# Kernel optimization log

Hardware: AMD Instinct MI355X
Metric: run time of the kernel (lower is better)

Reference implementation:

```python
import jax, jax.numpy as jnp
import numpy as np

N_EXPERTS = 256
N_GROUPS = 8
TOPK_GROUPS = 4
TOPK = 8
ROUTE_SCALE = 2.5
DIM = 7168


def setup_inputs() -> dict:
    key = jax.random.key(0)
    k1, k2, k3 = jax.random.split(key, 3)
    T = 16384
    x = jax.random.normal(k1, (T, DIM), dtype=jnp.float32)
    weight = jax.random.normal(k2, (N_EXPERTS, DIM), dtype=jnp.float32) * (1.0 / np.sqrt(DIM))
    bias = jax.random.normal(k3, (N_EXPERTS,), dtype=jnp.float32) * 0.1
    return {"x": x, "weight": weight, "bias": bias}


def reference(x, weight, bias):
    T = x.shape[0]
    # scores = sigmoid(x @ W^T)  -- sigmoid scoring path (score_func == 'sigmoid')
    scores = jax.nn.sigmoid(jnp.einsum('td,ed->te', x, weight))  # [T, E]
    original_scores = scores
    # bias-corrected scores used only for routing selection
    s = scores + bias[None, :]
    sg = s.reshape(T, N_GROUPS, N_EXPERTS // N_GROUPS)  # [T, G, E/G]
    # group score = sum of top-2 bias-corrected scores within each group
    top2, _ = jax.lax.top_k(sg, 2)
    group_scores = top2.sum(axis=-1)  # [T, G]
    _, gidx = jax.lax.top_k(group_scores, TOPK_GROUPS)  # [T, topk_groups]
    keep = jnp.zeros((T, N_GROUPS), dtype=bool).at[jnp.arange(T)[:, None], gidx].set(True)
    s_masked = jnp.where(keep[:, :, None], sg, -jnp.inf).reshape(T, N_EXPERTS)
    # top-k experts over group-masked, bias-corrected scores
    _, indices = jax.lax.top_k(s_masked, TOPK)  # [T, topk]
    # weights gathered from ORIGINAL (un-biased) sigmoid scores
    weights = jnp.take_along_axis(original_scores, indices, axis=1)  # [T, topk]
    weights = weights / weights.sum(axis=-1, keepdims=True)  # sigmoid renorm
    weights = weights * ROUTE_SCALE
    return weights, indices
```

## Files before the change

kernel.cpp:

```cpp
#include <hip/hip_runtime.h>
#include <math.h>

#define DIM_K 7168
#define NE 256
#define NG 8
#define GSZ 32
#define TOPKN 8
#define TOPKG 4

constexpr int BM = 32;
constexpr int BK = 16;
constexpr int LDK = BK + 4;

typedef __attribute__((ext_vector_type(4))) double dbl4;

constexpr int GEMM_BYTES  = (BM * LDK + NE * LDK) * 4;
constexpr int ROUTE_BYTES = (BM * (NE + 1) + NE) * 4;
constexpr int SMEM_BYTES  = ROUTE_BYTES > GEMM_BYTES ? ROUTE_BYTES : GEMM_BYTES;

__global__ __launch_bounds__(256, 2)
void gemm_sigmoid_route(const float* __restrict__ x,
                        const float* __restrict__ w,
                        const float* __restrict__ bias,
                        float* __restrict__ out_w,
                        float* __restrict__ out_i)
{
    __shared__ __align__(16) char smem[SMEM_BYTES];
    float (*As)[LDK] = (float (*)[LDK])smem;
    float (*Bs)[LDK] = (float (*)[LDK])(smem + BM * LDK * 4);

    const int tid  = threadIdx.x;
    const int wave = tid >> 6;
    const int lane = tid & 63;
    const int m_blk = blockIdx.x * BM;

    const int l15 = lane & 15;
    const int lk  = lane >> 4;
    const int e_base = wave * 64;

    const dbl4 zero = {0.0, 0.0, 0.0, 0.0};
    dbl4 acc[2][4];
#pragma unroll
    for (int i = 0; i < 2; ++i)
#pragma unroll
        for (int j = 0; j < 4; ++j) acc[i][j] = zero;

    const int srow = tid >> 2;
    const int sc4  = (tid & 3) * 4;

    const float* xa = x + (long)(m_blk + (srow & 31)) * DIM_K + sc4;
    const float* wb = w + (long)srow * DIM_K + sc4;

    float4 ra, rb0, rb1, rb2, rb3;
    if (tid < 128) ra = *(const float4*)xa;
    rb0 = *(const float4*)(wb);
    rb1 = *(const float4*)(wb + (long) 64 * DIM_K);
    rb2 = *(const float4*)(wb + (long)128 * DIM_K);
    rb3 = *(const float4*)(wb + (long)192 * DIM_K);

    for (int k0 = 0; k0 < DIM_K; k0 += BK) {
        if (tid < 128) *(float4*)&As[srow & 31][sc4] = ra;
        *(float4*)&Bs[srow      ][sc4] = rb0;
        *(float4*)&Bs[srow +  64][sc4] = rb1;
        *(float4*)&Bs[srow + 128][sc4] = rb2;
        *(float4*)&Bs[srow + 192][sc4] = rb3;
        __syncthreads();

        if (k0 + BK < DIM_K) {
            const int off = k0 + BK;
            if (tid < 128) ra = *(const float4*)(xa + off);
            rb0 = *(const float4*)(wb + off);
            rb1 = *(const float4*)(wb + off + (long) 64 * DIM_K);
            rb2 = *(const float4*)(wb + off + (long)128 * DIM_K);
            rb3 = *(const float4*)(wb + off + (long)192 * DIM_K);
        }

#pragma unroll
        for (int ks = 0; ks < BK; ks += 4) {
            const int kk = ks + lk;
            const double a0 = (double)As[l15     ][kk];
            const double a1 = (double)As[l15 + 16][kk];
            const double b0 = (double)Bs[e_base      + l15][kk];
            const double b1 = (double)Bs[e_base + 16 + l15][kk];
            const double b2 = (double)Bs[e_base + 32 + l15][kk];
            const double b3 = (double)Bs[e_base + 48 + l15][kk];
            acc[0][0] = __builtin_amdgcn_mfma_f64_16x16x4f64(a0, b0, acc[0][0], 0, 0, 0);
            acc[1][0] = __builtin_amdgcn_mfma_f64_16x16x4f64(a1, b0, acc[1][0], 0, 0, 0);
            acc[0][1] = __builtin_amdgcn_mfma_f64_16x16x4f64(a0, b1, acc[0][1], 0, 0, 0);
            acc[1][1] = __builtin_amdgcn_mfma_f64_16x16x4f64(a1, b1, acc[1][1], 0, 0, 0);
            acc[0][2] = __builtin_amdgcn_mfma_f64_16x16x4f64(a0, b2, acc[0][2], 0, 0, 0);
            acc[1][2] = __builtin_amdgcn_mfma_f64_16x16x4f64(a1, b2, acc[1][2], 0, 0, 0);
            acc[0][3] = __builtin_amdgcn_mfma_f64_16x16x4f64(a0, b3, acc[0][3], 0, 0, 0);
            acc[1][3] = __builtin_amdgcn_mfma_f64_16x16x4f64(a1, b3, acc[1][3], 0, 0, 0);
        }
        __syncthreads();
    }

    float (*sc)[NE + 1] = (float (*)[NE + 1])smem;
    float* bsh = (float*)(smem + BM * (NE + 1) * 4);

#pragma unroll
    for (int mi = 0; mi < 2; ++mi) {
#pragma unroll
        for (int j = 0; j < 4; ++j) {
#pragma unroll
            for (int r = 0; r < 4; ++r) {
                const int m = mi * 16 + r * 4 + lk;
                const int e = e_base + j * 16 + l15;
                sc[m][e] = (float)(1.0 / (1.0 + exp(-acc[mi][j][r])));
            }
        }
    }
    if (tid < 64) {
        const float4 bv = *(const float4*)(bias + tid * 4);
        bsh[tid * 4 + 0] = bv.x;
        bsh[tid * 4 + 1] = bv.y;
        bsh[tid * 4 + 2] = bv.z;
        bsh[tid * 4 + 3] = bv.w;
    }
    __syncthreads();

    if (tid < BM) {
        float* row = sc[tid];

        float gs[NG];
#pragma unroll
        for (int g = 0; g < NG; ++g) {
            float m1 = -3.0e38f, m2 = -3.0e38f;
            for (int j = 0; j < GSZ; ++j) {
                const int e = g * GSZ + j;
                const float v = __fadd_rn(row[e], bsh[e]);
                if (v > m1) { m2 = m1; m1 = v; }
                else if (v > m2) { m2 = v; }
            }
            gs[g] = __fadd_rn(m1, m2);
        }

        unsigned keep = 0;
#pragma unroll
        for (int r = 0; r < TOPKG; ++r) {
            float best = -3.0e38f; int bg = 0;
            for (int g = 0; g < NG; ++g)
                if (!((keep >> g) & 1u) && gs[g] > best) { best = gs[g]; bg = g; }
            keep |= 1u << bg;
        }

        float wv[TOPKN]; int iv[TOPKN];
        for (int r = 0; r < TOPKN; ++r) {
            float best = -3.0e38f; int bi = 0;
            for (int g = 0; g < NG; ++g) {
                if (!((keep >> g) & 1u)) continue;
                for (int j = 0; j < GSZ; ++j) {
                    const int e = g * GSZ + j;
                    const float v = __fadd_rn(row[e], bsh[e]);
                    if (v > best) { best = v; bi = e; }
                }
            }
            wv[r] = row[bi];
            iv[r] = bi;
            row[bi] = -3.0e38f;
        }

        const float s01 = __fadd_rn(wv[0], wv[1]);
        const float s23 = __fadd_rn(wv[2], wv[3]);
        const float s45 = __fadd_rn(wv[4], wv[5]);
        const float s67 = __fadd_rn(wv[6], wv[7]);
        const float wsum = __fadd_rn(__fadd_rn(s01, s23), __fadd_rn(s45, s67));

        const long token = m_blk + tid;
#pragma unroll
        for (int r = 0; r < TOPKN; ++r) {
            out_w[token * 8 + r] = __fmul_rn(__fdiv_rn(wv[r], wsum), 2.5f);
            out_i[token * 8 + r] = (float)iv[r];
        }
    }
}

extern "C" void kernel_launch(void* const* d_in, const int* in_sizes, int n_in,
                              void* d_out, int out_size, void* d_ws, size_t ws_size,
                              hipStream_t stream)
{
    const float* x    = (const float*)d_in[0];
    const float* w    = (const float*)d_in[1];
    const float* bias = (const float*)d_in[2];
    float* out = (float*)d_out;
    const int T = in_sizes[0] / DIM_K;

    gemm_sigmoid_route<<<dim3(T / BM), dim3(256), 0, stream>>>(
        x, w, bias, out, out + (long)T * TOPKN);
}
```

Before: 1.535 ms.

## Load GEMM fragments directly from global into registers, dropping LDS staging

The shared-memory staging of the x and W tiles is removed. Each lane now loads float4 MFMA operand fragments straight from global memory, with the k index permuted inside each 16-wide chunk so that A and B stay consistent. Register double-buffering prefetches the next chunk. This removes the two __syncthreads per k-step and the LDS write/read traffic. The cost is that all four waves load the same x rows redundantly, and the strided per-lane loads lean on L1/L2 caching instead of coalesced tile loads.

```diff
diff --git a/kernel.cpp b/kernel.cpp
--- a/kernel.cpp
+++ b/kernel.cpp
@@ -10,13 +10,39 @@
 
 constexpr int BM = 32;
 constexpr int BK = 16;
-constexpr int LDK = BK + 4;
+constexpr int NCH = DIM_K / BK;
 
 typedef __attribute__((ext_vector_type(4))) double dbl4;
 
-constexpr int GEMM_BYTES  = (BM * LDK + NE * LDK) * 4;
 constexpr int ROUTE_BYTES = (BM * (NE + 1) + NE) * 4;
-constexpr int SMEM_BYTES  = ROUTE_BYTES > GEMM_BYTES ? ROUTE_BYTES : GEMM_BYTES;
+
+
+#define MFMA_CLUSTER(A0, A1, B0, B1, B2, B3)                                   \
+    do {                                                                       \
+        const float af0[4] = {(A0).x, (A0).y, (A0).z, (A0).w};                 \
+        const float af1[4] = {(A1).x, (A1).y, (A1).z, (A1).w};                 \
+        const float bf0[4] = {(B0).x, (B0).y, (B0).z, (B0).w};                 \
+        const float bf1[4] = {(B1).x, (B1).y, (B1).z, (B1).w};                 \
+        const float bf2[4] = {(B2).x, (B2).y, (B2).z, (B2).w};                 \
+        const float bf3[4] = {(B3).x, (B3).y, (B3).z, (B3).w};                 \
+        _Pragma("unroll")                                                      \
+        for (int s = 0; s < 4; ++s) {                                          \
+            const double a0 = (double)af0[s];                                  \
+            const double a1 = (double)af1[s];                                  \
+            const double b0 = (double)bf0[s];                                  \
+            const double b1 = (double)bf1[s];                                  \
+            const double b2 = (double)bf2[s];                                  \
+            const double b3 = (double)bf3[s];                                  \
+            acc[0][0] = __builtin_amdgcn_mfma_f64_16x16x4f64(a0, b0, acc[0][0], 0, 0, 0); \
+            acc[1][0] = __builtin_amdgcn_mfma_f64_16x16x4f64(a1, b0, acc[1][0], 0, 0, 0); \
+            acc[0][1] = __builtin_amdgcn_mfma_f64_16x16x4f64(a0, b1, acc[0][1], 0, 0, 0); \
+            acc[1][1] = __builtin_amdgcn_mfma_f64_16x16x4f64(a1, b1, acc[1][1], 0, 0, 0); \
+            acc[0][2] = __builtin_amdgcn_mfma_f64_16x16x4f64(a0, b2, acc[0][2], 0, 0, 0); \
+            acc[1][2] = __builtin_amdgcn_mfma_f64_16x16x4f64(a1, b2, acc[1][2], 0, 0, 0); \
+            acc[0][3] = __builtin_amdgcn_mfma_f64_16x16x4f64(a0, b3, acc[0][3], 0, 0, 0); \
+            acc[1][3] = __builtin_amdgcn_mfma_f64_16x16x4f64(a1, b3, acc[1][3], 0, 0, 0); \
+        }                                                                      \
+    } while (0)
 
 __global__ __launch_bounds__(256, 2)
 void gemm_sigmoid_route(const float* __restrict__ x,
@@ -25,9 +51,7 @@
                         float* __restrict__ out_w,
                         float* __restrict__ out_i)
 {
-    __shared__ __align__(16) char smem[SMEM_BYTES];
-    float (*As)[LDK] = (float (*)[LDK])smem;
-    float (*Bs)[LDK] = (float (*)[LDK])(smem + BM * LDK * 4);
+    __shared__ __align__(16) char smem[ROUTE_BYTES];
 
     const int tid  = threadIdx.x;
     const int wave = tid >> 6;
@@ -36,6 +60,7 @@
 
     const int l15 = lane & 15;
     const int lk  = lane >> 4;
+    const int klo = lk * 4;
     const int e_base = wave * 64;
 
     const dbl4 zero = {0.0, 0.0, 0.0, 0.0};
@@ -45,56 +70,35 @@
 #pragma unroll
         for (int j = 0; j < 4; ++j) acc[i][j] = zero;
 
-    const int srow = tid >> 2;
-    const int sc4  = (tid & 3) * 4;
+    const float* pa0 = x + (long)(m_blk + l15     ) * DIM_K + klo;
+    const float* pa1 = x + (long)(m_blk + 16 + l15) * DIM_K + klo;
+    const float* pb0 = w + (long)(e_base      + l15) * DIM_K + klo;
+    const float* pb1 = pb0 + (long)16 * DIM_K;
+    const float* pb2 = pb0 + (long)32 * DIM_K;
+    const float* pb3 = pb0 + (long)48 * DIM_K;
 
-    const float* xa = x + (long)(m_blk + (srow & 31)) * DIM_K + sc4;
-    const float* wb = w + (long)srow * DIM_K + sc4;
+    float4 a0c = *(const float4*)pa0;
+    float4 a1c = *(const float4*)pa1;
+    float4 b0c = *(const float4*)pb0;
+    float4 b1c = *(const float4*)pb1;
+    float4 b2c = *(const float4*)pb2;
+    float4 b3c = *(const float4*)pb3;
 
-    float4 ra, rb0, rb1, rb2, rb3;
-    if (tid < 128) ra = *(const float4*)xa;
-    rb0 = *(const float4*)(wb);
-    rb1 = *(const float4*)(wb + (long) 64 * DIM_K);
-    rb2 = *(const float4*)(wb + (long)128 * DIM_K);
-    rb3 = *(const float4*)(wb + (long)192 * DIM_K);
+    for (int t = 0; t < NCH - 1; ++t) {
+        const int off = (t + 1) * BK;
+        const float4 a0n = *(const float4*)(pa0 + off);
+        const float4 a1n = *(const float4*)(pa1 + off);
+        const float4 b0n = *(const float4*)(pb0 + off);
+        const float4 b1n = *(const float4*)(pb1 + off);
+        const float4 b2n = *(const float4*)(pb2 + off);
+        const float4 b3n = *(const float4*)(pb3 + off);
 
-    for (int k0 = 0; k0 < DIM_K; k0 += BK) {
-        if (tid < 128) *(float4*)&As[srow & 31][sc4] = ra;
-        *(float4*)&Bs[srow      ][sc4] = rb0;
-        *(float4*)&Bs[srow +  64][sc4] = rb1;
-        *(float4*)&Bs[srow + 128][sc4] = rb2;
-        *(float4*)&Bs[srow + 192][sc4] = rb3;
-        __syncthreads();
+        MFMA_CLUSTER(a0c, a1c, b0c, b1c, b2c, b3c);
 
-        if (k0 + BK < DIM_K) {
-            const int off = k0 + BK;
-            if (tid < 128) ra = *(const float4*)(xa + off);
-            rb0 = *(const float4*)(wb + off);
-            rb1 = *(const float4*)(wb + off + (long) 64 * DIM_K);
-            rb2 = *(const float4*)(wb + off + (long)128 * DIM_K);
-            rb3 = *(const float4*)(wb + off + (long)192 * DIM_K);
-        }
-
-#pragma unroll
-        for (int ks = 0; ks < BK; ks += 4) {
-            const int kk = ks + lk;
-            const double a0 = (double)As[l15     ][kk];
-            const double a1 = (double)As[l15 + 16][kk];
-            const double b0 = (double)Bs[e_base      + l15][kk];
-            const double b1 = (double)Bs[e_base + 16 + l15][kk];
-            const double b2 = (double)Bs[e_base + 32 + l15][kk];
-            const double b3 = (double)Bs[e_base + 48 + l15][kk];
-            acc[0][0] = __builtin_amdgcn_mfma_f64_16x16x4f64(a0, b0, acc[0][0], 0, 0, 0);
-            acc[1][0] = __builtin_amdgcn_mfma_f64_16x16x4f64(a1, b0, acc[1][0], 0, 0, 0);
-            acc[0][1] = __builtin_amdgcn_mfma_f64_16x16x4f64(a0, b1, acc[0][1], 0, 0, 0);
-            acc[1][1] = __builtin_amdgcn_mfma_f64_16x16x4f64(a1, b1, acc[1][1], 0, 0, 0);
-            acc[0][2] = __builtin_amdgcn_mfma_f64_16x16x4f64(a0, b2, acc[0][2], 0, 0, 0);
-            acc[1][2] = __builtin_amdgcn_mfma_f64_16x16x4f64(a1, b2, acc[1][2], 0, 0, 0);
-            acc[0][3] = __builtin_amdgcn_mfma_f64_16x16x4f64(a0, b3, acc[0][3], 0, 0, 0);
-            acc[1][3] = __builtin_amdgcn_mfma_f64_16x16x4f64(a1, b3, acc[1][3], 0, 0, 0);
-        }
-        __syncthreads();
+        a0c = a0n; a1c = a1n;
+        b0c = b0n; b1c = b1n; b2c = b2n; b3c = b3n;
     }
+    MFMA_CLUSTER(a0c, a1c, b0c, b1c, b2c, b3c);
 
     float (*sc)[NE + 1] = (float (*)[NE + 1])smem;
     float* bsh = (float*)(smem + BM * (NE + 1) * 4);
```

Result: faster. 1.440 ms (-6.2%).
